# Kernel optimization log

Hardware: AMD Instinct MI355X
Metric: run time of the kernel (lower is better)

Reference implementation:

```python
import jax, jax.numpy as jnp
import numpy as np

N_NODES = 50000
D_MODEL = 128
N_EDGES = 600000
HIDDEN = 128
EDGE_FEAT = 2 * D_MODEL + 2  # 258


def setup_inputs() -> dict:
    key = jax.random.key(0)
    k = jax.random.split(key, 8)
    H = jax.random.normal(k[0], (N_NODES, D_MODEL), dtype=jnp.float32)
    edge_index = jax.random.randint(k[1], (2, N_EDGES), 0, N_NODES, dtype=jnp.int64)
    S_e = jax.random.uniform(k[2], (N_EDGES,), dtype=jnp.float32)
    F_e = jax.random.uniform(k[3], (N_EDGES,), dtype=jnp.float32)
    W1 = jax.random.normal(k[4], (EDGE_FEAT, HIDDEN), dtype=jnp.float32) * (1.0 / np.sqrt(EDGE_FEAT))
    b1 = jnp.zeros((HIDDEN,), dtype=jnp.float32)
    W2 = jax.random.normal(k[5], (HIDDEN, 1), dtype=jnp.float32) * (1.0 / np.sqrt(HIDDEN))
    b2 = jnp.zeros((1,), dtype=jnp.float32)
    return {"H": H, "edge_index": edge_index, "S_e": S_e, "F_e": F_e,
            "W1": W1, "b1": b1, "W2": W2, "b2": b2}


def reference(H, edge_index, S_e, F_e, W1, b1, W2, b2):
    # Gather endpoint node features: [E, D]
    H_u = H[edge_index[0]]
    H_v = H[edge_index[1]]
    H_diff = jnp.abs(H_u - H_v)
    H_prod = H_u * H_v
    # [E, 2D+2]
    edge_features = jnp.concatenate(
        [H_diff, H_prod, S_e[:, None], F_e[:, None]], axis=1)
    # 2-layer MLP with SiLU (dropout is identity in eval mode)
    h = jax.nn.silu(edge_features @ W1 + b1)
    a_e = (h @ W2 + b2)[:, 0]  # [E]
    return a_e
```

## Files before the change

### kernel.cpp

```cpp
#include <hip/hip_runtime.h>


typedef _Float16       half8   __attribute__((ext_vector_type(8)));
typedef _Float16       half4v  __attribute__((ext_vector_type(4)));
typedef unsigned short ushort8 __attribute__((ext_vector_type(8)));
typedef float          f32x4   __attribute__((ext_vector_type(4)));

#define NSEG       8
#define W1T_STRIDE 288

__device__ __forceinline__ float silu_f(float x) {
    return x / (1.0f + __expf(-x));
}

__device__ __forceinline__ void canon(int u, int v, int& a, int& b) {
    const int sw = (u ^ v) & 1;
    a = sw ? v : u;
    b = sw ? u : v;
}


__global__ __launch_bounds__(256)
void cvt_hist_kernel(const float* __restrict__ H, _Float16* __restrict__ Hh,
                     int n4, const int* __restrict__ eidx,
                     int* __restrict__ hist, int E, int ASZ, int BBINS) {
    int i = blockIdx.x * blockDim.x + threadIdx.x;
    if (i < n4) {
        const float4 f = ((const float4*)H)[i];
        half4v h;
        h[0] = (_Float16)f.x; h[1] = (_Float16)f.y;
        h[2] = (_Float16)f.z; h[3] = (_Float16)f.w;
        ((half4v*)Hh)[i] = h;
    }
    if (i < E) {
        int a, b;
        canon(eidx[i], eidx[E + i], a, b);
        atomicAdd(&hist[(a / ASZ) * BBINS + (b >> 3)], 1);
    }
}

__global__ __launch_bounds__(256)
void scan_kernel(int* __restrict__ hist, int* __restrict__ bsum,
                 int NB, int nb1, int* __restrict__ flag,
                 int* __restrict__ vbs, int BBINS, int E) {
    __shared__ int s[256];
    __shared__ int lastBlk;
    const int t = threadIdx.x;
    const int i = blockIdx.x * 256 + t;
    const int v = (i < NB) ? hist[i] : 0;
    s[t] = v;
    __syncthreads();
    for (int off = 1; off < 256; off <<= 1) {
        const int x = (t >= off) ? s[t - off] : 0;
        __syncthreads();
        s[t] += x;
        __syncthreads();
    }
    if (i < NB) hist[i] = s[t] - v;
    if (t == 255) bsum[blockIdx.x] = s[255];
    __threadfence();
    if (t == 0) lastBlk = (atomicAdd(flag, 1) == (int)gridDim.x - 1);
    __syncthreads();
    if (!lastBlk) return;
    const int bv = (t < nb1) ? atomicAdd(&bsum[t], 0) : 0;
    s[t] = bv;
    __syncthreads();
    for (int off = 1; off < 256; off <<= 1) {
        const int x = (t >= off) ? s[t - off] : 0;
        __syncthreads();
        s[t] += x;
        __syncthreads();
    }
    if (t < nb1) bsum[t] = s[t] - bv;
    __syncthreads();
    if (t < NSEG) {
        const int idx = t * BBINS;
        vbs[t] = atomicAdd(&hist[idx], 0) + bsum[idx >> 8];
    } else if (t == NSEG) {
        vbs[NSEG] = E;
    }
}

__global__ __launch_bounds__(256)
void scatter_kernel(const int* __restrict__ eidx, const float* __restrict__ Se,
                    const float* __restrict__ Fe, int* __restrict__ ofs,
                    const int* __restrict__ bsum,
                    int4* __restrict__ recs, int E, int ASZ, int BBINS) {
    int e = blockIdx.x * blockDim.x + threadIdx.x;
    if (e < E) {
        int a, b;
        canon(eidx[e], eidx[E + e], a, b);
        const int key = (a / ASZ) * BBINS + (b >> 3);
        const int pos = atomicAdd(&ofs[key], 1) + bsum[key >> 8];
        _Float16 sh = (_Float16)Se[e];
        _Float16 fh = (_Float16)Fe[e];
        unsigned pk = (unsigned)*(unsigned short*)&sh
                    | ((unsigned)*(unsigned short*)&fh << 16);
        recs[pos] = make_int4(a, b, e, (int)pk);
    }
}


__device__ __forceinline__ void stage_w1(const float* __restrict__ W1,
                                         const float* __restrict__ b1,
                                         _Float16* __restrict__ w1t, int tid) {
    const int n = tid & 127;
    const int g = tid >> 7;
    #pragma unroll
    for (int i = 0; i < 5; ++i) {
        const int kb = g + (i << 3);
        if (kb < 32) {
            half8 tmp;
            #pragma unroll
            for (int j = 0; j < 8; ++j) {
                const int kp  = (kb << 3) + j;
                const int c   = kp >> 5;
                const int k32 = kp & 31;
                const int src = ((c & 1) << 7) + ((c >> 1) << 5) + k32;
                tmp[j] = (_Float16)W1[src * 128 + n];
            }
            *(half8*)&w1t[n * W1T_STRIDE + ((kb ^ (n & 7)) << 3)] = tmp;
        } else if (kb < 36) {
            const int k32b = (kb - 32) << 3;
            half8 tmp;
            #pragma unroll
            for (int j = 0; j < 8; ++j) {
                const int k32 = k32b + j;
                float v = 0.f;
                if (k32 == 0)      v = W1[32768 + n];
                else if (k32 == 1) v = W1[32896 + n];
                else if (k32 == 2) v = b1[n];
                tmp[j] = (_Float16)v;
            }
            *(half8*)&w1t[n * W1T_STRIDE + (kb << 3)] = tmp;
        }
    }
}


__device__ __forceinline__ void edge_tile16(
    const _Float16* __restrict__ Hh, const int4* __restrict__ recs,
    const _Float16* __restrict__ w1t,
    const f32x4* __restrict__ w2r, float b2v, float* __restrict__ out,
    int ebase, int elim, int q, int cb, int swz)
{
    const int e = min(ebase + cb, elim - 1);
    const int4 r = recs[e];
    const int a = r.x, b = r.y;
    const unsigned pk = (unsigned)r.w;
    const unsigned short sl = (unsigned short)(pk & 0xFFFF);
    const unsigned short fl = (unsigned short)(pk >> 16);

    const _Float16* up = Hh + (size_t)a * 128;
    const _Float16* vp = Hh + (size_t)b * 128;

    f32x4 acc[8];
    #pragma unroll
    for (int t = 0; t < 8; ++t) acc[t] = (f32x4){0.f, 0.f, 0.f, 0.f};

    #pragma unroll
    for (int c8 = 0; c8 < 4; ++c8) {
        const half8 u8 = *(const half8*)(up + (c8 << 5) + (q << 3));
        const half8 v8 = *(const half8*)(vp + (c8 << 5) + (q << 3));
        half8 d8 = u8 - v8;
        ushort8 du = *(ushort8*)&d8;
        du = du & (unsigned short)0x7FFF;
        const half8 ae = *(half8*)&du;
        const half8 ao = u8 * v8;

        const int kb0 = ((c8 << 3) + q) ^ swz;
        const int kb1 = ((c8 << 3) + 4 + q) ^ swz;
        #pragma unroll
        for (int t = 0; t < 8; ++t) {
            const half8 b0 = *(const half8*)&w1t[((t << 4) + cb) * W1T_STRIDE + (kb0 << 3)];
            acc[t] = __builtin_amdgcn_mfma_f32_16x16x32_f16(b0, ae, acc[t], 0, 0, 0);
        }
        #pragma unroll
        for (int t = 0; t < 8; ++t) {
            const half8 b1f = *(const half8*)&w1t[((t << 4) + cb) * W1T_STRIDE + (kb1 << 3)];
            acc[t] = __builtin_amdgcn_mfma_f32_16x16x32_f16(b1f, ao, acc[t], 0, 0, 0);
        }
    }

    half8 aE;
    #pragma unroll
    for (int j = 0; j < 8; ++j) aE[j] = (_Float16)0.f;
    if (q == 0) {
        aE[0] = *(const _Float16*)&sl;
        aE[1] = *(const _Float16*)&fl;
        aE[2] = (_Float16)1.0f;
    }
    #pragma unroll
    for (int t = 0; t < 8; ++t) {
        const half8 bE = *(const half8*)&w1t[((t << 4) + cb) * W1T_STRIDE + ((32 + q) << 3)];
        acc[t] = __builtin_amdgcn_mfma_f32_16x16x32_f16(bE, aE, acc[t], 0, 0, 0);
    }

    float rs = 0.f;
    #pragma unroll
    for (int t = 0; t < 8; ++t) {
        const f32x4 av = acc[t];
        const f32x4 wv = w2r[t];
        #pragma unroll
        for (int rr = 0; rr < 4; ++rr)
            rs += silu_f(av[rr]) * wv[rr];
    }
    rs += __shfl_xor(rs, 16);
    rs += __shfl_xor(rs, 32);

    if (q == 0 && ebase + cb < elim) out[r.z] = rs + b2v;
}


__global__ __launch_bounds__(1024, 2)
void edgegate_seg(const _Float16* __restrict__ Hh,
                  const int4*  __restrict__ recs,
                  const int*   __restrict__ vbs,
                  int*         __restrict__ ctr,
                  const float* __restrict__ W1,
                  const float* __restrict__ b1,
                  const float* __restrict__ W2,
                  const float* __restrict__ b2,
                  float*       __restrict__ out)
{
    __shared__ _Float16 w1t[128 * W1T_STRIDE];
    __shared__ int tkt[2];
    const int tid = threadIdx.x;
    stage_w1(W1, b1, w1t, tid);

    int xcd;
    asm volatile("s_getreg_b32 %0, hwreg(HW_REG_XCC_ID)" : "=s"(xcd));
    xcd &= (NSEG - 1);

    const int lane = tid & 63;
    const int wave = tid >> 6;
    const int q    = lane >> 4;
    const int cb   = lane & 15;
    const int swz  = cb & 7;
    const float b2v = b2[0];
    f32x4 w2r[8];
    #pragma unroll
    for (int t = 0; t < 8; ++t)
        w2r[t] = *(const f32x4*)&W2[(t << 4) + (q << 2)];

    int p = 0;
    for (int sidx = 0; sidx < NSEG; ++sidx) {
        const int seg = (xcd + sidx) & (NSEG - 1);
        const int vs  = vbs[seg];
        const int ve  = vbs[seg + 1];
        const int ner = ve - vs;
        if (ner <= 0) continue;
        const int Tt = (ner + 255) >> 8;

        __syncthreads();
        if (tid == 0) tkt[p] = atomicAdd(&ctr[seg], 1);
        __syncthreads();
        int t0 = tkt[p];
        while (t0 < Tt) {
            const int pn = p ^ 1;
            if (tid == 0) tkt[pn] = atomicAdd(&ctr[seg], 1);
            const int ebase = vs + (t0 << 8) + (wave << 4);
            edge_tile16(Hh, recs, w1t, w2r, b2v, out, ebase, ve, q, cb, swz);
            __syncthreads();
            p = pn;
            t0 = tkt[p];
        }
    }
}


__global__ __launch_bounds__(1024, 2)
void edgegate_fb(const float* __restrict__ H,
                 const _Float16* __restrict__ Hh,
                 const int*   __restrict__ eidx,
                 const float* __restrict__ Se,
                 const float* __restrict__ Fe,
                 const float* __restrict__ W1,
                 const float* __restrict__ b1,
                 const float* __restrict__ W2,
                 const float* __restrict__ b2,
                 float*       __restrict__ out,
                 int E, int ntiles, int useF16)
{
    __shared__ _Float16 w1t[128 * W1T_STRIDE];
    const int tid = threadIdx.x;
    stage_w1(W1, b1, w1t, tid);

    const int lane = tid & 63;
    const int wave = tid >> 6;
    const int q    = lane >> 4;
    const int cb   = lane & 15;
    const int swz  = cb & 7;
    const float b2v = b2[0];
    f32x4 w2r[8];
    #pragma unroll
    for (int t = 0; t < 8; ++t)
        w2r[t] = *(const f32x4*)&W2[(t << 4) + (q << 2)];

    __syncthreads();

    for (int tile = blockIdx.x; tile < ntiles; tile += gridDim.x) {
        const int ebase = tile * 256 + wave * 16;
        int e = ebase + cb;
        if (e >= E) e = E - 1;
        const int u = eidx[e];
        const int v = eidx[E + e];
        const float sfe = Se[e];
        const float ffe = Fe[e];

        f32x4 acc[8];
        #pragma unroll
        for (int t = 0; t < 8; ++t) acc[t] = (f32x4){0.f, 0.f, 0.f, 0.f};

        #pragma unroll
        for (int c8 = 0; c8 < 4; ++c8) {
            half8 ae, ao;
            if (useF16) {
                const _Float16* up = Hh + (size_t)u * 128;
                const _Float16* vp = Hh + (size_t)v * 128;
                const half8 u8 = *(const half8*)(up + (c8 << 5) + (q << 3));
                const half8 v8 = *(const half8*)(vp + (c8 << 5) + (q << 3));
                half8 d8 = u8 - v8;
                ushort8 du = *(ushort8*)&d8;
                du = du & (unsigned short)0x7FFF;
                ae = *(half8*)&du;
                ao = u8 * v8;
            } else {
                const float* up = H + (size_t)u * 128;
                const float* vp = H + (size_t)v * 128;
                #pragma unroll
                for (int j = 0; j < 8; ++j) {
                    const float uu = up[(c8 << 5) + (q << 3) + j];
                    const float vv = vp[(c8 << 5) + (q << 3) + j];
                    ae[j] = (_Float16)fabsf(uu - vv);
                    ao[j] = (_Float16)(uu * vv);
                }
            }
            const int kb0 = ((c8 << 3) + q) ^ swz;
            const int kb1 = ((c8 << 3) + 4 + q) ^ swz;
            #pragma unroll
            for (int t = 0; t < 8; ++t) {
                const half8 b0 = *(const half8*)&w1t[((t << 4) + cb) * W1T_STRIDE + (kb0 << 3)];
                acc[t] = __builtin_amdgcn_mfma_f32_16x16x32_f16(b0, ae, acc[t], 0, 0, 0);
            }
            #pragma unroll
            for (int t = 0; t < 8; ++t) {
                const half8 b1f = *(const half8*)&w1t[((t << 4) + cb) * W1T_STRIDE + (kb1 << 3)];
                acc[t] = __builtin_amdgcn_mfma_f32_16x16x32_f16(b1f, ao, acc[t], 0, 0, 0);
            }
        }

        half8 aE;
        #pragma unroll
        for (int j = 0; j < 8; ++j) aE[j] = (_Float16)0.f;
        if (q == 0) {
            aE[0] = (_Float16)sfe;
            aE[1] = (_Float16)ffe;
            aE[2] = (_Float16)1.0f;
        }
        #pragma unroll
        for (int t = 0; t < 8; ++t) {
            const half8 bE = *(const half8*)&w1t[((t << 4) + cb) * W1T_STRIDE + ((32 + q) << 3)];
            acc[t] = __builtin_amdgcn_mfma_f32_16x16x32_f16(bE, aE, acc[t], 0, 0, 0);
        }

        float rs = 0.f;
        #pragma unroll
        for (int t = 0; t < 8; ++t) {
            const f32x4 av = acc[t];
            const f32x4 wv = w2r[t];
            #pragma unroll
            for (int rr = 0; rr < 4; ++rr)
                rs += silu_f(av[rr]) * wv[rr];
        }
        rs += __shfl_xor(rs, 16);
        rs += __shfl_xor(rs, 32);

        if (q == 0 && ebase + cb < E) out[ebase + cb] = rs + b2v;
    }
}


static inline size_t align256(size_t x) { return (x + 255) & ~(size_t)255; }

extern "C" void kernel_launch(void* const* d_in, const int* in_sizes, int n_in,
                              void* d_out, int out_size, void* d_ws, size_t ws_size,
                              hipStream_t stream)
{
    const float* H    = (const float*)d_in[0];
    const int*   eidx = (const int*)  d_in[1];
    const float* Se   = (const float*)d_in[2];
    const float* Fe   = (const float*)d_in[3];
    const float* W1   = (const float*)d_in[4];
    const float* b1   = (const float*)d_in[5];
    const float* W2   = (const float*)d_in[6];
    const float* b2   = (const float*)d_in[7];
    float* out = (float*)d_out;

    const int nH     = in_sizes[0];
    const int nNodes = nH / 128;
    const int E      = in_sizes[2];
    const int n4     = nH / 4;
    const int ntiles = (E + 255) / 256;

    const int ASZ   = (nNodes + NSEG - 1) / NSEG;
    const int BBINS = (nNodes + 7) >> 3;
    const int NB    = NSEG * BBINS;
    const int nb1   = (NB + 255) / 256;

    const size_t hhB    = (size_t)nH * sizeof(_Float16);
    const size_t off_g  = align256(hhB);
    const size_t off_bs = align256(off_g + (size_t)(NB + 16) * 4);
    const size_t off_vb = align256(off_bs + 256 * 4);
    const size_t off_r  = align256(off_vb + 16 * 4);
    const size_t need   = off_r + (size_t)E * sizeof(int4);

    if (ws_size >= need && nb1 <= 256) {
        _Float16* Hh   = (_Float16*)((char*)d_ws);
        int*      hist = (int*)     ((char*)d_ws + off_g);
        int*      ctr  = hist + NB;
        int*      flag = hist + NB + 8;
        int*      bsum = (int*)     ((char*)d_ws + off_bs);
        int*      vbs  = (int*)     ((char*)d_ws + off_vb);
        int4*     recs = (int4*)    ((char*)d_ws + off_r);

        const int ncvh = (n4 > E) ? n4 : E;
        hipMemsetAsync(hist, 0, (size_t)(NB + 16) * sizeof(int), stream);
        hipLaunchKernelGGL(cvt_hist_kernel, dim3((ncvh + 255) / 256), dim3(256),
                           0, stream, H, Hh, n4, eidx, hist, E, ASZ, BBINS);
        hipLaunchKernelGGL(scan_kernel, dim3(nb1), dim3(256), 0, stream,
                           hist, bsum, NB, nb1, flag, vbs, BBINS, E);
        hipLaunchKernelGGL(scatter_kernel, dim3((E + 255) / 256), dim3(256),
                           0, stream, eidx, Se, Fe, hist, bsum, recs,
                           E, ASZ, BBINS);
        hipLaunchKernelGGL(edgegate_seg, dim3(256), dim3(1024), 0, stream,
                           Hh, recs, vbs, ctr, W1, b1, W2, b2, out);
    } else if (ws_size >= hhB) {
        _Float16* Hh = (_Float16*)d_ws;
        const int grid = (256 < ntiles) ? 256 : ntiles;
        hipLaunchKernelGGL(cvt_hist_kernel, dim3((n4 + 255) / 256), dim3(256),
                           0, stream, H, Hh, n4, eidx, (int*)nullptr, 0, 1, 1);
        hipLaunchKernelGGL(edgegate_fb, dim3(grid), dim3(1024), 0, stream,
                           H, Hh, eidx, Se, Fe, W1, b1, W2, b2, out, E, ntiles, 1);
    } else {
        const int grid = (256 < ntiles) ? 256 : ntiles;
        hipLaunchKernelGGL(edgegate_fb, dim3(grid), dim3(1024), 0, stream,
                           H, (const _Float16*)nullptr, eidx, Se, Fe, W1, b1, W2, b2,
                           out, E, ntiles, 0);
    }
}
```

Measured before the change: 278.1 us.

## Fuse histogram, scan and scatter preprocessing into one persistent kernel with grid barriers

Replaces the memset, convert/histogram, scan and scatter kernel launches with a single persistent prep kernel of 768 blocks that separates its phases with software grid barriers built on atomic counters. This is meant to remove launch gaps and the per-kernel drain between the small preprocessing stages. The cost is spin-waiting at four grid-wide barriers, and the scheme relies on all 768 blocks being resident at once to avoid deadlock. Grid-stride loops replace the one-thread-per-element launches.

```diff
diff --git a/kernel.cpp b/kernel.cpp
--- a/kernel.cpp
+++ b/kernel.cpp
@@ -19,11 +19,105 @@
     b = sw ? u : v;
 }
 
+__device__ __forceinline__ void gbar(int* cnt, int target) {
+    __syncthreads();
+    if (threadIdx.x == 0) {
+        __threadfence();
+        atomicAdd(cnt, 1);
+        while (__hip_atomic_load(cnt, __ATOMIC_RELAXED,
+                                 __HIP_MEMORY_SCOPE_AGENT) < target)
+            __builtin_amdgcn_s_sleep(2);
+    }
+    __syncthreads();
+}
+
+
+__global__ __launch_bounds__(256, 4)
+void prep_kernel(const float* __restrict__ H, _Float16* __restrict__ Hh,
+                 int n4, const int* __restrict__ eidx,
+                 const float* __restrict__ Se, const float* __restrict__ Fe,
+                 int* __restrict__ hist, int* __restrict__ bsum,
+                 int* __restrict__ vbs, int4* __restrict__ recs,
+                 int* __restrict__ bar,
+                 int E, int ASZ, int BBINS, int NB, int nb1)
+{
+    __shared__ int s[256];
+    const int tid  = threadIdx.x;
+    const int gtid = blockIdx.x * 256 + tid;
+    const int gsz  = gridDim.x * 256;
+    const int G    = gridDim.x;
+
+    for (int i = gtid; i < NB + 8; i += gsz) hist[i] = 0;
+    gbar(&bar[0], G);
+
+    for (int i = gtid; i < n4; i += gsz) {
+        const float4 f = ((const float4*)H)[i];
+        half4v h;
+        h[0] = (_Float16)f.x; h[1] = (_Float16)f.y;
+        h[2] = (_Float16)f.z; h[3] = (_Float16)f.w;
+        ((half4v*)Hh)[i] = h;
+    }
+    for (int e = gtid; e < E; e += gsz) {
+        int a, b;
+        canon(eidx[e], eidx[E + e], a, b);
+        atomicAdd(&hist[(a / ASZ) * BBINS + (b >> 3)], 1);
+    }
+    gbar(&bar[1], G);
+
+    if (blockIdx.x < nb1) {
+        const int i = blockIdx.x * 256 + tid;
+        const int v = (i < NB) ? atomicAdd(&hist[i], 0) : 0;
+        s[tid] = v;
+        __syncthreads();
+        for (int off = 1; off < 256; off <<= 1) {
+            const int x = (tid >= off) ? s[tid - off] : 0;
+            __syncthreads();
+            s[tid] += x;
+            __syncthreads();
+        }
+        if (i < NB) hist[i] = s[tid] - v;
+        if (tid == 255) bsum[blockIdx.x] = s[255];
+    }
+    gbar(&bar[2], G);
+
+    if (blockIdx.x == 0) {
+        const int v = (tid < nb1) ? atomicAdd(&bsum[tid], 0) : 0;
+        s[tid] = v;
+        __syncthreads();
+        for (int off = 1; off < 256; off <<= 1) {
+            const int x = (tid >= off) ? s[tid - off] : 0;
+            __syncthreads();
+            s[tid] += x;
+            __syncthreads();
+        }
+        if (tid < nb1) bsum[tid] = s[tid] - v;
+        __syncthreads();
+        if (tid < NSEG) {
+            const int idx = tid * BBINS;
+            vbs[tid] = atomicAdd(&hist[idx], 0) + bsum[idx >> 8];
+        } else if (tid == NSEG) {
+            vbs[NSEG] = E;
+        }
+    }
+    gbar(&bar[3], G);
+
+    s[tid] = (tid < nb1) ? atomicAdd(&bsum[tid], 0) : 0;
+    __syncthreads();
+    for (int e = gtid; e < E; e += gsz) {
+        int a, b;
+        canon(eidx[e], eidx[E + e], a, b);
+        const int key = (a / ASZ) * BBINS + (b >> 3);
+        const int pos = atomicAdd(&hist[key], 1) + s[key >> 8];
+        _Float16 sh = (_Float16)Se[e];
+        _Float16 fh = (_Float16)Fe[e];
+        unsigned pk = (unsigned)*(unsigned short*)&sh
+                    | ((unsigned)*(unsigned short*)&fh << 16);
+        recs[pos] = make_int4(a, b, e, (int)pk);
+    }
+}
 
 __global__ __launch_bounds__(256)
-void cvt_hist_kernel(const float* __restrict__ H, _Float16* __restrict__ Hh,
-                     int n4, const int* __restrict__ eidx,
-                     int* __restrict__ hist, int E, int ASZ, int BBINS) {
+void cvt_kernel(const float* __restrict__ H, _Float16* __restrict__ Hh, int n4) {
     int i = blockIdx.x * blockDim.x + threadIdx.x;
     if (i < n4) {
         const float4 f = ((const float4*)H)[i];
@@ -31,72 +125,6 @@
         h[0] = (_Float16)f.x; h[1] = (_Float16)f.y;
         h[2] = (_Float16)f.z; h[3] = (_Float16)f.w;
         ((half4v*)Hh)[i] = h;
-    }
-    if (i < E) {
-        int a, b;
-        canon(eidx[i], eidx[E + i], a, b);
-        atomicAdd(&hist[(a / ASZ) * BBINS + (b >> 3)], 1);
-    }
-}
-
-__global__ __launch_bounds__(256)
-void scan_kernel(int* __restrict__ hist, int* __restrict__ bsum,
-                 int NB, int nb1, int* __restrict__ flag,
-                 int* __restrict__ vbs, int BBINS, int E) {
-    __shared__ int s[256];
-    __shared__ int lastBlk;
-    const int t = threadIdx.x;
-    const int i = blockIdx.x * 256 + t;
-    const int v = (i < NB) ? hist[i] : 0;
-    s[t] = v;
-    __syncthreads();
-    for (int off = 1; off < 256; off <<= 1) {
-        const int x = (t >= off) ? s[t - off] : 0;
-        __syncthreads();
-        s[t] += x;
-        __syncthreads();
-    }
-    if (i < NB) hist[i] = s[t] - v;
-    if (t == 255) bsum[blockIdx.x] = s[255];
-    __threadfence();
-    if (t == 0) lastBlk = (atomicAdd(flag, 1) == (int)gridDim.x - 1);
-    __syncthreads();
-    if (!lastBlk) return;
-    const int bv = (t < nb1) ? atomicAdd(&bsum[t], 0) : 0;
-    s[t] = bv;
-    __syncthreads();
-    for (int off = 1; off < 256; off <<= 1) {
-        const int x = (t >= off) ? s[t - off] : 0;
-        __syncthreads();
-        s[t] += x;
-        __syncthreads();
-    }
-    if (t < nb1) bsum[t] = s[t] - bv;
-    __syncthreads();
-    if (t < NSEG) {
-        const int idx = t * BBINS;
-        vbs[t] = atomicAdd(&hist[idx], 0) + bsum[idx >> 8];
-    } else if (t == NSEG) {
-        vbs[NSEG] = E;
-    }
-}
-
-__global__ __launch_bounds__(256)
-void scatter_kernel(const int* __restrict__ eidx, const float* __restrict__ Se,
-                    const float* __restrict__ Fe, int* __restrict__ ofs,
-                    const int* __restrict__ bsum,
-                    int4* __restrict__ recs, int E, int ASZ, int BBINS) {
-    int e = blockIdx.x * blockDim.x + threadIdx.x;
-    if (e < E) {
-        int a, b;
-        canon(eidx[e], eidx[E + e], a, b);
-        const int key = (a / ASZ) * BBINS + (b >> 3);
-        const int pos = atomicAdd(&ofs[key], 1) + bsum[key >> 8];
-        _Float16 sh = (_Float16)Se[e];
-        _Float16 fh = (_Float16)Fe[e];
-        unsigned pk = (unsigned)*(unsigned short*)&sh
-                    | ((unsigned)*(unsigned short*)&fh << 16);
-        recs[pos] = make_int4(a, b, e, (int)pk);
     }
 }
 
@@ -419,27 +447,22 @@
         _Float16* Hh   = (_Float16*)((char*)d_ws);
         int*      hist = (int*)     ((char*)d_ws + off_g);
         int*      ctr  = hist + NB;
-        int*      flag = hist + NB + 8;
+        int*      bar  = hist + NB + 8;
         int*      bsum = (int*)     ((char*)d_ws + off_bs);
         int*      vbs  = (int*)     ((char*)d_ws + off_vb);
         int4*     recs = (int4*)    ((char*)d_ws + off_r);
 
-        const int ncvh = (n4 > E) ? n4 : E;
-        hipMemsetAsync(hist, 0, (size_t)(NB + 16) * sizeof(int), stream);
-        hipLaunchKernelGGL(cvt_hist_kernel, dim3((ncvh + 255) / 256), dim3(256),
-                           0, stream, H, Hh, n4, eidx, hist, E, ASZ, BBINS);
-        hipLaunchKernelGGL(scan_kernel, dim3(nb1), dim3(256), 0, stream,
-                           hist, bsum, NB, nb1, flag, vbs, BBINS, E);
-        hipLaunchKernelGGL(scatter_kernel, dim3((E + 255) / 256), dim3(256),
-                           0, stream, eidx, Se, Fe, hist, bsum, recs,
-                           E, ASZ, BBINS);
+        hipMemsetAsync(bar, 0, 4 * sizeof(int), stream);
+        hipLaunchKernelGGL(prep_kernel, dim3(768), dim3(256), 0, stream,
+                           H, Hh, n4, eidx, Se, Fe, hist, bsum, vbs, recs,
+                           bar, E, ASZ, BBINS, NB, nb1);
         hipLaunchKernelGGL(edgegate_seg, dim3(256), dim3(1024), 0, stream,
                            Hh, recs, vbs, ctr, W1, b1, W2, b2, out);
     } else if (ws_size >= hhB) {
         _Float16* Hh = (_Float16*)d_ws;
         const int grid = (256 < ntiles) ? 256 : ntiles;
-        hipLaunchKernelGGL(cvt_hist_kernel, dim3((n4 + 255) / 256), dim3(256),
-                           0, stream, H, Hh, n4, eidx, (int*)nullptr, 0, 1, 1);
+        hipLaunchKernelGGL(cvt_kernel, dim3((n4 + 255) / 256), dim3(256),
+                           0, stream, H, Hh, n4);
         hipLaunchKernelGGL(edgegate_fb, dim3(grid), dim3(1024), 0, stream,
                            H, Hh, eidx, Se, Fe, W1, b1, W2, b2, out, E, ntiles, 1);
     } else {
```

Result: slower. 463.6 us (+66.7%).

## Switch edge MLP to 32x32x16 MFMA tiles with 512-thread blocks

Applied to the files above, without the earlier changes.

The main segmented edge kernel now uses 32x32x16 f16 MFMA, so each wave handles 32 edges against 128 hidden units in four accumulators instead of 16 edges with eight 16x16 tiles. This raises data reuse per LDS read of W1 and cuts the number of MFMA issues. Blocks shrink to 512 threads with a 512-block grid, W2 is staged in LDS rather than held in registers, and a plain conversion kernel replaces the histogram-capable one on the fallback path. Costs include higher accumulator register pressure and a different LDS access pattern for W1.

```diff
diff --git a/kernel.cpp b/kernel.cpp
--- a/kernel.cpp
+++ b/kernel.cpp
@@ -5,6 +5,7 @@
 typedef _Float16       half4v  __attribute__((ext_vector_type(4)));
 typedef unsigned short ushort8 __attribute__((ext_vector_type(8)));
 typedef float          f32x4   __attribute__((ext_vector_type(4)));
+typedef float          f32x16  __attribute__((ext_vector_type(16)));
 
 #define NSEG       8
 #define W1T_STRIDE 288
@@ -100,10 +101,57 @@
     }
 }
 
-
-__device__ __forceinline__ void stage_w1(const float* __restrict__ W1,
-                                         const float* __restrict__ b1,
-                                         _Float16* __restrict__ w1t, int tid) {
+__global__ __launch_bounds__(256)
+void cvt_kernel(const float* __restrict__ H, _Float16* __restrict__ Hh, int n4) {
+    int i = blockIdx.x * blockDim.x + threadIdx.x;
+    if (i < n4) {
+        const float4 f = ((const float4*)H)[i];
+        half4v h;
+        h[0] = (_Float16)f.x; h[1] = (_Float16)f.y;
+        h[2] = (_Float16)f.z; h[3] = (_Float16)f.w;
+        ((half4v*)Hh)[i] = h;
+    }
+}
+
+
+__device__ __forceinline__ void stage_w1_512(const float* __restrict__ W1,
+                                             const float* __restrict__ b1,
+                                             _Float16* __restrict__ w1t, int tid) {
+    const int n = tid & 127;
+    const int g = tid >> 7;
+    #pragma unroll
+    for (int i = 0; i < 9; ++i) {
+        const int kb = g + (i << 2);
+        half8 tmp;
+        if (kb < 32) {
+            #pragma unroll
+            for (int j = 0; j < 8; ++j) {
+                const int kp  = (kb << 3) + j;
+                const int c   = kp >> 5;
+                const int k32 = kp & 31;
+                const int src = ((c & 1) << 7) + ((c >> 1) << 5) + k32;
+                tmp[j] = (_Float16)W1[src * 128 + n];
+            }
+            *(half8*)&w1t[n * W1T_STRIDE + ((kb ^ (n & 7)) << 3)] = tmp;
+        } else {
+            const int k32b = (kb - 32) << 3;
+            #pragma unroll
+            for (int j = 0; j < 8; ++j) {
+                const int k32 = k32b + j;
+                float v = 0.f;
+                if (k32 == 0)      v = W1[32768 + n];
+                else if (k32 == 1) v = W1[32896 + n];
+                else if (k32 == 2) v = b1[n];
+                tmp[j] = (_Float16)v;
+            }
+            *(half8*)&w1t[n * W1T_STRIDE + (kb << 3)] = tmp;
+        }
+    }
+}
+
+__device__ __forceinline__ void stage_w1_1024(const float* __restrict__ W1,
+                                              const float* __restrict__ b1,
+                                              _Float16* __restrict__ w1t, int tid) {
     const int n = tid & 127;
     const int g = tid >> 7;
     #pragma unroll
@@ -138,81 +186,7 @@
 }
 
 
-__device__ __forceinline__ void edge_tile16(
-    const _Float16* __restrict__ Hh, const int4* __restrict__ recs,
-    const _Float16* __restrict__ w1t,
-    const f32x4* __restrict__ w2r, float b2v, float* __restrict__ out,
-    int ebase, int elim, int q, int cb, int swz)
-{
-    const int e = min(ebase + cb, elim - 1);
-    const int4 r = recs[e];
-    const int a = r.x, b = r.y;
-    const unsigned pk = (unsigned)r.w;
-    const unsigned short sl = (unsigned short)(pk & 0xFFFF);
-    const unsigned short fl = (unsigned short)(pk >> 16);
-
-    const _Float16* up = Hh + (size_t)a * 128;
-    const _Float16* vp = Hh + (size_t)b * 128;
-
-    f32x4 acc[8];
-    #pragma unroll
-    for (int t = 0; t < 8; ++t) acc[t] = (f32x4){0.f, 0.f, 0.f, 0.f};
-
-    #pragma unroll
-    for (int c8 = 0; c8 < 4; ++c8) {
-        const half8 u8 = *(const half8*)(up + (c8 << 5) + (q << 3));
-        const half8 v8 = *(const half8*)(vp + (c8 << 5) + (q << 3));
-        half8 d8 = u8 - v8;
-        ushort8 du = *(ushort8*)&d8;
-        du = du & (unsigned short)0x7FFF;
-        const half8 ae = *(half8*)&du;
-        const half8 ao = u8 * v8;
-
-        const int kb0 = ((c8 << 3) + q) ^ swz;
-        const int kb1 = ((c8 << 3) + 4 + q) ^ swz;
-        #pragma unroll
-        for (int t = 0; t < 8; ++t) {
-            const half8 b0 = *(const half8*)&w1t[((t << 4) + cb) * W1T_STRIDE + (kb0 << 3)];
-            acc[t] = __builtin_amdgcn_mfma_f32_16x16x32_f16(b0, ae, acc[t], 0, 0, 0);
-        }
-        #pragma unroll
-        for (int t = 0; t < 8; ++t) {
-            const half8 b1f = *(const half8*)&w1t[((t << 4) + cb) * W1T_STRIDE + (kb1 << 3)];
-            acc[t] = __builtin_amdgcn_mfma_f32_16x16x32_f16(b1f, ao, acc[t], 0, 0, 0);
-        }
-    }
-
-    half8 aE;
-    #pragma unroll
-    for (int j = 0; j < 8; ++j) aE[j] = (_Float16)0.f;
-    if (q == 0) {
-        aE[0] = *(const _Float16*)&sl;
-        aE[1] = *(const _Float16*)&fl;
-        aE[2] = (_Float16)1.0f;
-    }
-    #pragma unroll
-    for (int t = 0; t < 8; ++t) {
-        const half8 bE = *(const half8*)&w1t[((t << 4) + cb) * W1T_STRIDE + ((32 + q) << 3)];
-        acc[t] = __builtin_amdgcn_mfma_f32_16x16x32_f16(bE, aE, acc[t], 0, 0, 0);
-    }
-
-    float rs = 0.f;
-    #pragma unroll
-    for (int t = 0; t < 8; ++t) {
-        const f32x4 av = acc[t];
-        const f32x4 wv = w2r[t];
-        #pragma unroll
-        for (int rr = 0; rr < 4; ++rr)
-            rs += silu_f(av[rr]) * wv[rr];
-    }
-    rs += __shfl_xor(rs, 16);
-    rs += __shfl_xor(rs, 32);
-
-    if (q == 0 && ebase + cb < elim) out[r.z] = rs + b2v;
-}
-
-
-__global__ __launch_bounds__(1024, 2)
+__global__ __launch_bounds__(512, 2)
 void edgegate_seg(const _Float16* __restrict__ Hh,
                   const int4*  __restrict__ recs,
                   const int*   __restrict__ vbs,
@@ -224,9 +198,11 @@
                   float*       __restrict__ out)
 {
     __shared__ _Float16 w1t[128 * W1T_STRIDE];
+    __shared__ float    w2l[128];
     __shared__ int tkt[2];
     const int tid = threadIdx.x;
-    stage_w1(W1, b1, w1t, tid);
+    stage_w1_512(W1, b1, w1t, tid);
+    if (tid < 32) ((float4*)w2l)[tid] = ((const float4*)W2)[tid];
 
     int xcd;
     asm volatile("s_getreg_b32 %0, hwreg(HW_REG_XCC_ID)" : "=s"(xcd));
@@ -234,14 +210,10 @@
 
     const int lane = tid & 63;
     const int wave = tid >> 6;
-    const int q    = lane >> 4;
-    const int cb   = lane & 15;
-    const int swz  = cb & 7;
+    const int col  = lane & 31;
+    const int hi   = lane >> 5;
+    const int swz  = lane & 7;
     const float b2v = b2[0];
-    f32x4 w2r[8];
-    #pragma unroll
-    for (int t = 0; t < 8; ++t)
-        w2r[t] = *(const f32x4*)&W2[(t << 4) + (q << 2)];
 
     int p = 0;
     for (int sidx = 0; sidx < NSEG; ++sidx) {
@@ -259,8 +231,88 @@
         while (t0 < Tt) {
             const int pn = p ^ 1;
             if (tid == 0) tkt[pn] = atomicAdd(&ctr[seg], 1);
-            const int ebase = vs + (t0 << 8) + (wave << 4);
-            edge_tile16(Hh, recs, w1t, w2r, b2v, out, ebase, ve, q, cb, swz);
+
+            const int ebase = vs + (t0 << 8) + (wave << 5);
+            const int e = min(ebase + col, ve - 1);
+            const int4 r = recs[e];
+            const _Float16* up = Hh + (size_t)r.x * 128;
+            const _Float16* vp = Hh + (size_t)r.y * 128;
+
+            f32x16 acc[4];
+            #pragma unroll
+            for (int t = 0; t < 4; ++t) {
+                #pragma unroll
+                for (int j = 0; j < 16; ++j) acc[t][j] = 0.f;
+            }
+
+            #pragma unroll
+            for (int cp = 0; cp < 4; ++cp) {
+                const int dbase = (cp << 5) + (hi << 3);
+                const half8 u0 = *(const half8*)(up + dbase);
+                const half8 v0 = *(const half8*)(vp + dbase);
+                const half8 u1 = *(const half8*)(up + dbase + 16);
+                const half8 v1 = *(const half8*)(vp + dbase + 16);
+                half8 d0 = u0 - v0;
+                half8 d1 = u1 - v1;
+                ushort8 x0 = *(ushort8*)&d0; x0 = x0 & (unsigned short)0x7FFF;
+                ushort8 x1 = *(ushort8*)&d1; x1 = x1 & (unsigned short)0x7FFF;
+                const half8 ae0 = *(half8*)&x0;
+                const half8 ae1 = *(half8*)&x1;
+                const half8 ao0 = u0 * v0;
+                const half8 ao1 = u1 * v1;
+
+                const int kbe0 = ((cp << 3) + 0 + hi) ^ swz;
+                const int kbe1 = ((cp << 3) + 2 + hi) ^ swz;
+                const int kbo0 = ((cp << 3) + 4 + hi) ^ swz;
+                const int kbo1 = ((cp << 3) + 6 + hi) ^ swz;
+                #pragma unroll
+                for (int t = 0; t < 4; ++t) {
+                    const _Float16* wr = &w1t[((t << 5) + col) * W1T_STRIDE];
+                    const half8 we0 = *(const half8*)&wr[kbe0 << 3];
+                    acc[t] = __builtin_amdgcn_mfma_f32_32x32x16_f16(we0, ae0, acc[t], 0, 0, 0);
+                    const half8 we1 = *(const half8*)&wr[kbe1 << 3];
+                    acc[t] = __builtin_amdgcn_mfma_f32_32x32x16_f16(we1, ae1, acc[t], 0, 0, 0);
+                    const half8 wo0 = *(const half8*)&wr[kbo0 << 3];
+                    acc[t] = __builtin_amdgcn_mfma_f32_32x32x16_f16(wo0, ao0, acc[t], 0, 0, 0);
+                    const half8 wo1 = *(const half8*)&wr[kbo1 << 3];
+                    acc[t] = __builtin_amdgcn_mfma_f32_32x32x16_f16(wo1, ao1, acc[t], 0, 0, 0);
+                }
+            }
+
+            {
+                const unsigned pk = (unsigned)r.w;
+                const unsigned short sl = (unsigned short)(pk & 0xFFFF);
+                const unsigned short fl = (unsigned short)(pk >> 16);
+                half8 aE;
+                #pragma unroll
+                for (int j = 0; j < 8; ++j) aE[j] = (_Float16)0.f;
+                if (hi == 0) {
+                    aE[0] = *(const _Float16*)&sl;
+                    aE[1] = *(const _Float16*)&fl;
+                    aE[2] = (_Float16)1.0f;
+                }
+                #pragma unroll
+                for (int t = 0; t < 4; ++t) {
+                    const half8 wE = *(const half8*)&w1t[((t << 5) + col) * W1T_STRIDE + ((32 + hi) << 3)];
+                    acc[t] = __builtin_amdgcn_mfma_f32_32x32x16_f16(wE, aE, acc[t], 0, 0, 0);
+                }
+            }
+
+            float rs = 0.f;
+            #pragma unroll
+            for (int t = 0; t < 4; ++t) {
+                #pragma unroll
+                for (int g = 0; g < 4; ++g) {
+                    const f32x4 wv = *(const f32x4*)&w2l[(t << 5) + (g << 3) + (hi << 2)];
+                    #pragma unroll
+                    for (int rr = 0; rr < 4; ++rr)
+                        rs += silu_f(acc[t][(g << 2) + rr]) * wv[rr];
+                }
+            }
+            rs += __shfl_xor(rs, 32);
+
+            if (hi == 0 && ebase + col < ve) out[r.z] = rs + b2v;
+
             __syncthreads();
             p = pn;
             t0 = tkt[p];
@@ -284,7 +336,7 @@
 {
     __shared__ _Float16 w1t[128 * W1T_STRIDE];
     const int tid = threadIdx.x;
-    stage_w1(W1, b1, w1t, tid);
+    stage_w1_1024(W1, b1, w1t, tid);
 
     const int lane = tid & 63;
     const int wave = tid >> 6;
@@ -433,13 +485,13 @@
         hipLaunchKernelGGL(scatter_kernel, dim3((E + 255) / 256), dim3(256),
                            0, stream, eidx, Se, Fe, hist, bsum, recs,
                            E, ASZ, BBINS);
-        hipLaunchKernelGGL(edgegate_seg, dim3(256), dim3(1024), 0, stream,
+        hipLaunchKernelGGL(edgegate_seg, dim3(512), dim3(512), 0, stream,
                            Hh, recs, vbs, ctr, W1, b1, W2, b2, out);
     } else if (ws_size >= hhB) {
         _Float16* Hh = (_Float16*)d_ws;
         const int grid = (256 < ntiles) ? 256 : ntiles;
-        hipLaunchKernelGGL(cvt_hist_kernel, dim3((n4 + 255) / 256), dim3(256),
-                           0, stream, H, Hh, n4, eidx, (int*)nullptr, 0, 1, 1);
+        hipLaunchKernelGGL(cvt_kernel, dim3((n4 + 255) / 256), dim3(256),
+                           0, stream, H, Hh, n4);
         hipLaunchKernelGGL(edgegate_fb, dim3(grid), dim3(1024), 0, stream,
                            H, Hh, eidx, Se, Fe, W1, b1, W2, b2, out, E, ntiles, 1);
     } else {
```

New measurement: 300.9 us. 1.08x slower.
